# Performance work log

Measured on AMD Instinct MI355X. Metric: run time of the kernel, lower is better.

Reference implementation:

```python
import jax, jax.numpy as jnp
import numpy as np

B, L, D = 4, 1024, 1024
H = 16
HD = D // H
SCALE = HD ** -0.5
LOCAL_WINDOW = 32
HALF = LOCAL_WINDOW // 2
TEMP = 1.0
PATTERN_TEMP = 1.0
THRESHOLD = 0.1
SPARSITY_RATIO = 0.3
# k for learned sparse topk (eval mode, static given L)
EFF = min(SPARSITY_RATIO, 1.0 - 10.0 / L)
K_TOP = max(1, min(L, int(L * (1.0 - EFF))))


def setup_inputs() -> dict:
    key = jax.random.key(0)
    ks = jax.random.split(key, 16)
    def xavier(k, shape, gain=1.0):
        fan_in, fan_out = shape[1], shape[0]
        a = gain * np.sqrt(6.0 / (fan_in + fan_out))
        return jax.random.uniform(k, shape, jnp.float32, -a, a)
    return {
        'x': jax.random.normal(ks[0], (B, L, D), jnp.float32),
        'w_qkv': xavier(ks[1], (3 * D, D), gain=1.0 / np.sqrt(2.0)),
        'w_proj': xavier(ks[2], (D, D)),
        'b_proj': jnp.zeros((D,), jnp.float32),
        'ps_w1': xavier(ks[3], (D, D), gain=0.5),
        'ps_b1': jnp.zeros((D,), jnp.float32),
        'ln_g': jnp.ones((D,), jnp.float32),
        'ln_b': jnp.zeros((D,), jnp.float32),
        'ps_w2': xavier(ks[4], (D // 2, D), gain=0.5),
        'ps_b2': jnp.zeros((D // 2,), jnp.float32),
        'ps_w3': xavier(ks[5], (3, D // 2), gain=0.5),
        'ps_b3': jnp.zeros((3,), jnp.float32),
        'pattern_bias': jnp.array([0.05, 0.0, -0.05], jnp.float32),
        'sparse_w': jax.random.normal(ks[6], (H, 1, 1), jnp.float32) * 0.1 + 1.0,
        'sparse_b': jnp.zeros((H, 1, 1), jnp.float32),
    }


def _forward(x, w_qkv, w_proj, b_proj, ps_w1, ps_b1, ln_g, ln_b,
             ps_w2, ps_b2, ps_w3, ps_b3, pattern_bias, sparse_w, sparse_b):
    qkv = (x @ w_qkv.T).reshape(B, L, 3, H, HD)
    qkv = jnp.transpose(qkv, (2, 0, 3, 1, 4))  # [3,B,H,L,HD]
    q, k, v = qkv[0], qkv[1], qkv[2]
    scores = jnp.einsum('bhid,bhjd->bhij', q, k) * SCALE  # [B,H,L,L]

    # pattern selector on pooled features
    pooled = (jnp.mean(x, axis=1) + jnp.max(x, axis=1)) / 2.0  # [B,D]
    h = pooled @ ps_w1.T + ps_b1
    mu = jnp.mean(h, axis=-1, keepdims=True)
    var = jnp.mean((h - mu) ** 2, axis=-1, keepdims=True)
    h = (h - mu) / jnp.sqrt(var + 1e-5) * ln_g + ln_b
    h = jax.nn.gelu(h, approximate=False)
    h = jax.nn.gelu(h @ ps_w2.T + ps_b2, approximate=False)
    logits = h @ ps_w3.T + ps_b3 + pattern_bias  # [B,3]
    pw = jax.nn.softmax(logits / PATTERN_TEMP, axis=-1)  # [B,3]

    # learned sparse mask via per-head affine + topk scatter
    s2 = scores * jnp.abs(sparse_w)[None] + sparse_b[None]  # [B,H,L,L]
    _, topk_idx = jax.lax.top_k(s2, K_TOP)  # [B,H,L,K]
    bi = jnp.arange(B)[:, None, None, None]
    hi = jnp.arange(H)[None, :, None, None]
    li = jnp.arange(L)[None, None, :, None]
    sparse_mask = jnp.zeros_like(scores).at[bi, hi, li, topk_idx].set(1.0)

    # local sliding-window mask |i-j| <= HALF
    i = jnp.arange(L)
    local = (jnp.abs(i[:, None] - i[None, :]) <= HALF).astype(jnp.float32)  # [L,L]

    combined = (pw[:, 0, None, None, None] * local[None, None]
                + pw[:, 1, None, None, None]
                + pw[:, 2, None, None, None] * sparse_mask)
    binary = combined > THRESHOLD
    scores = jnp.where(binary, scores, -jnp.inf)

    # fallback: rows fully masked attend only to themselves (score 0)
    all_masked = ~jnp.any(binary, axis=-1)  # [B,H,L]
    eye = jnp.eye(L, dtype=bool)
    scores = jnp.where(all_masked[..., None] & eye[None, None], 0.0, scores)

    attn = jax.nn.softmax(scores / TEMP, axis=-1)
    out = jnp.einsum('bhij,bhjd->bhid', attn, v)  # [B,H,L,HD]
    out = jnp.transpose(out, (0, 2, 1, 3)).reshape(B, L, D)
    return out @ w_proj.T + b_proj


def reference(x, w_qkv, w_proj, b_proj, ps_w1, ps_b1, ln_g, ln_b,
              ps_w2, ps_b2, ps_w3, ps_b3, pattern_bias, sparse_w, sparse_b):
    return _forward(x, w_qkv, w_proj, b_proj, ps_w1, ps_b1, ln_g, ln_b,
                    ps_w2, ps_b2, ps_w3, ps_b3, pattern_bias, sparse_w, sparse_b)
```

## Files before the change

### kernel.cpp

```cpp
#include <hip/hip_runtime.h>
#include <math.h>

#define KTOP_ 716
#define SCALE_ 0.125f
#define QSCALE_ 0.1803368801111731f
#define LN2_ 0.6931471805599453f

#define WAIT_VMCNT(n) asm volatile("s_waitcnt vmcnt(" #n ")" ::: "memory")
static __device__ inline void SBAR() {
  __builtin_amdgcn_sched_barrier(0);
  __builtin_amdgcn_s_barrier();
  __builtin_amdgcn_sched_barrier(0);
}

typedef float f4v __attribute__((ext_vector_type(4)));
typedef short s8v __attribute__((ext_vector_type(8)));
typedef __bf16 bf8v __attribute__((ext_vector_type(8)));

static __device__ inline unsigned short f2bf(float f) {
  unsigned u = __float_as_uint(f);
  u += 0x7fffu + ((u >> 16) & 1u);
  return (unsigned short)(u >> 16);
}
static __device__ inline unsigned short f2bfn(float f) {
  union { __bf16 b; unsigned short u; } cv;
  cv.b = (__bf16)f;
  return cv.u;
}
static __device__ inline float bf2f(unsigned short h) {
  return __uint_as_float((unsigned)h << 16);
}
static __device__ inline f4v mfma16(s8v a, s8v b, f4v c) {
  union { s8v s; bf8v b; } ua, ub;
  ua.s = a; ub.s = b;
  return __builtin_amdgcn_mfma_f32_16x16x32_bf16(ua.b, ub.b, c, 0, 0, 0);
}
static __device__ inline void gload16(const unsigned short* g, unsigned short* lbase) {
  __builtin_amdgcn_global_load_lds(
      (const __attribute__((address_space(1))) unsigned int*)g,
      (__attribute__((address_space(3))) unsigned int*)lbase, 16, 0, 0);
}

__global__ __launch_bounds__(256) void pool1(const float* __restrict__ x,
                                             float* __restrict__ psum,
                                             float* __restrict__ pmax,
                                             unsigned short* __restrict__ xs) {
  int bid = blockIdx.x;
  int b = bid >> 6, sl = bid & 63;
  int t = threadIdx.x;
  float s[4] = {0.f, 0.f, 0.f, 0.f};
  float m[4] = {-INFINITY, -INFINITY, -INFINITY, -INFINITY};
  const float* xb = x + ((size_t)b << 20) + (size_t)sl * 16 * 1024;
  unsigned short* xo = xs + ((size_t)(b * 1024 + sl * 16)) * 1024;
  for (int l = 0; l < 16; ++l) {
    #pragma unroll
    for (int dg = 0; dg < 4; ++dg) {
      float v = xb[l * 1024 + dg * 256 + t];
      s[dg] += v;
      m[dg] = fmaxf(m[dg], v);
      xo[(size_t)l * 1024 + dg * 256 + t] = f2bfn(v);
    }
  }
  #pragma unroll
  for (int dg = 0; dg < 4; ++dg) {
    psum[(size_t)bid * 1024 + dg * 256 + t] = s[dg];
    pmax[(size_t)bid * 1024 + dg * 256 + t] = m[dg];
  }
}

__global__ __launch_bounds__(256) void ps_gemv1(const float* __restrict__ psum,
                                                const float* __restrict__ pmax,
                                                const float* __restrict__ w1,
                                                const float* __restrict__ b1,
                                                float* __restrict__ h1) {
  __shared__ float pool_s[1024];
  int bid = blockIdx.x;
  int b = bid >> 4, og = bid & 15;
  int t = threadIdx.x;
  #pragma unroll
  for (int i = 0; i < 4; ++i) {
    int d = t + 256 * i;
    float s = 0.f, m = -INFINITY;
    #pragma unroll 8
    for (int sl = 0; sl < 64; ++sl) {
      s += psum[((size_t)b * 64 + sl) * 1024 + d];
      m = fmaxf(m, pmax[((size_t)b * 64 + sl) * 1024 + d]);
    }
    pool_s[d] = (s * (1.0f / 1024.0f) + m) * 0.5f;
  }
  __syncthreads();
  int ol = t >> 2, ks = t & 3;
  int o = og * 64 + ol;
  const float4* wr = (const float4*)(w1 + (size_t)o * 1024 + ks * 256);
  const float4* pp = (const float4*)(&pool_s[ks * 256]);
  float acc = 0.f;
  #pragma unroll 8
  for (int j = 0; j < 64; ++j) {
    float4 a = wr[j], p = pp[j];
    acc += a.x * p.x + a.y * p.y + a.z * p.z + a.w * p.w;
  }
  acc += __shfl_xor(acc, 1, 64);
  acc += __shfl_xor(acc, 2, 64);
  if (ks == 0) h1[b * 1024 + o] = acc + b1[o];
}

__global__ __launch_bounds__(256) void ps_gemv2(const float* __restrict__ h1,
                                                const float* __restrict__ lng,
                                                const float* __restrict__ lnb,
                                                const float* __restrict__ w2,
                                                const float* __restrict__ b2,
                                                float* __restrict__ h2) {
  __shared__ float hs[1024];
  __shared__ float red[256];
  int bid = blockIdx.x;
  int b = bid >> 3, og = bid & 7;
  int t = threadIdx.x;
  const float* hb = h1 + b * 1024;
  float v0[4];
  float ls = 0.f;
  #pragma unroll
  for (int i = 0; i < 4; ++i) { v0[i] = hb[t + 256 * i]; ls += v0[i]; }
  red[t] = ls; __syncthreads();
  for (int s = 128; s > 0; s >>= 1) { if (t < s) red[t] += red[t + s]; __syncthreads(); }
  float mean = red[0] * (1.0f / 1024.0f);
  __syncthreads();
  float lq = 0.f;
  #pragma unroll
  for (int i = 0; i < 4; ++i) { float dv = v0[i] - mean; lq += dv * dv; }
  red[t] = lq; __syncthreads();
  for (int s = 128; s > 0; s >>= 1) { if (t < s) red[t] += red[t + s]; __syncthreads(); }
  float rstd = 1.0f / sqrtf(red[0] * (1.0f / 1024.0f) + 1e-5f);
  #pragma unroll
  for (int i = 0; i < 4; ++i) {
    float v = (v0[i] - mean) * rstd * lng[t + 256 * i] + lnb[t + 256 * i];
    hs[t + 256 * i] = 0.5f * v * (1.0f + erff(v * 0.70710678118654752f));
  }
  __syncthreads();
  int ol = t >> 2, ks = t & 3;
  int o = og * 64 + ol;
  const float4* wr = (const float4*)(w2 + (size_t)o * 1024 + ks * 256);
  const float4* pp = (const float4*)(&hs[ks * 256]);
  float acc = 0.f;
  #pragma unroll 8
  for (int j = 0; j < 64; ++j) {
    float4 a = wr[j], p = pp[j];
    acc += a.x * p.x + a.y * p.y + a.z * p.z + a.w * p.w;
  }
  acc += __shfl_xor(acc, 1, 64);
  acc += __shfl_xor(acc, 2, 64);
  if (ks == 0) {
    float v = acc + b2[o];
    h2[b * 512 + o] = 0.5f * v * (1.0f + erff(v * 0.70710678118654752f));
  }
}

__global__ __launch_bounds__(256) void ps_logits(const float* __restrict__ h2,
                                                 const float* __restrict__ w3,
                                                 const float* __restrict__ b3,
                                                 const float* __restrict__ pb,
                                                 int* __restrict__ meta) {
  __shared__ float red[256];
  int b = blockIdx.x, t = threadIdx.x;
  float lgv[3];
  for (int c = 0; c < 3; ++c) {
    float p = 0.f;
    for (int i = t; i < 512; i += 256) p += h2[b * 512 + i] * w3[c * 512 + i];
    red[t] = p; __syncthreads();
    for (int s = 128; s > 0; s >>= 1) { if (t < s) red[t] += red[t + s]; __syncthreads(); }
    lgv[c] = red[0] + b3[c] + pb[c];
    __syncthreads();
  }
  if (t == 0) {
    float mx = fmaxf(lgv[0], fmaxf(lgv[1], lgv[2]));
    float e0 = __expf(lgv[0] - mx), e1 = __expf(lgv[1] - mx), e2 = __expf(lgv[2] - mx);
    float inv = 1.0f / (e0 + e1 + e2);
    float p0 = e0 * inv, p1 = e1 * inv, p2 = e2 * inv;
    float c00 = p1;
    float c10 = p0 + p1;
    float c01 = p1 + p2;
    float c11 = (p0 + p1) + p2;
    int t00 = c00 > 0.1f, t10 = c10 > 0.1f, t01 = c01 > 0.1f, t11 = c11 > 0.1f;
    meta[b * 8 + 0] = t00;
    meta[b * 8 + 1] = t10;
    meta[b * 8 + 2] = t01;
    meta[b * 8 + 3] = t11;
    meta[b * 8 + 4] = (t00 != t01) || (t10 != t11);
  }
}

__global__ __launch_bounds__(256) void prep_w(const float* __restrict__ w_qkv,
                                              const float* __restrict__ w_proj,
                                              unsigned short* __restrict__ wqs,
                                              unsigned short* __restrict__ wps) {
  int i = blockIdx.x * 256 + threadIdx.x;
  const float* src;
  unsigned short* dst;
  int idx;
  if (i < 786432) { src = w_qkv; dst = wqs; idx = i; }
  else            { src = w_proj; dst = wps; idx = i - 786432; }
  float4 v = ((const float4*)src)[idx];
  ushort4 o;
  o.x = f2bfn(v.x); o.y = f2bfn(v.y); o.z = f2bfn(v.z); o.w = f2bfn(v.w);
  *(ushort4*)(dst + (size_t)idx * 4) = o;
}

template <int MODE, int TM>
__global__ __launch_bounds__(256) void gemm_sp(
    const unsigned short* __restrict__ A, const unsigned short* __restrict__ B,
    const float* __restrict__ bias,
    unsigned short* __restrict__ qxo, unsigned short* __restrict__ kxo,
    unsigned short* __restrict__ vxo,
    float* __restrict__ out, int Nb) {
  constexpr int MFR = TM / 32;
  __shared__ unsigned short AsmA[TM * 64];
  __shared__ unsigned short AsmB[TM * 64];
  __shared__ unsigned short BsmA[128 * 64];
  __shared__ unsigned short BsmB[128 * 64];

  int bid = blockIdx.x;
  int bm, bn;
  if (MODE == 0) {
    int xcd = bid & 7, idx = bid >> 3;
    int rb = (xcd >> 1) * 8, cb = (xcd & 1) * 12;
    int r, c;
    if (idx < 64) { r = idx & 7; c = idx >> 3; }
    else          { int j = idx - 64; r = j & 7; c = 8 + (j >> 3); }
    bm = rb + r; bn = cb + c;
  } else {
    int cpx = gridDim.x >> 3;
    int g = (bid & 7) * cpx + (bid >> 3);
    bm = g / Nb; bn = g % Nb;
  }
  size_t row0 = (size_t)bm * TM, col0 = (size_t)bn * 128;

  int tid = threadIdx.x, lane = tid & 63, wv = tid >> 6;
  int wm = (wv >> 1) * (MFR * 16), wn = (wv & 1) << 6;
  int rowg = lane >> 4, colc = lane & 15;

  f4v acc[MFR][4];
  #pragma unroll
  for (int mf = 0; mf < MFR; ++mf)
    #pragma unroll
    for (int nf = 0; nf < 4; ++nf) acc[mf][nf] = (f4v){0.f, 0.f, 0.f, 0.f};

  const unsigned short* Abase = A + row0 * 1024;
  const unsigned short* Bbase = B + col0 * 1024;

  auto STAGE = [&](int kb, unsigned short* Ad, unsigned short* Bd) {
    #pragma unroll
    for (int p = 0; p < TM / 32; ++p) {
      int idx = p * 256 + tid;
      int row = idx >> 3;
      int sc = (idx & 7) ^ (row & 7);
      gload16(Abase + (size_t)row * 1024 + kb + sc * 8,
              Ad + (size_t)(p * 256 + wv * 64) * 8);
    }
    #pragma unroll
    for (int p = 0; p < 4; ++p) {
      int idx = p * 256 + tid;
      int row = idx >> 3;
      int sc = (idx & 7) ^ (row & 7);
      gload16(Bbase + (size_t)row * 1024 + kb + sc * 8,
              Bd + (size_t)(p * 256 + wv * 64) * 8);
    }
  };

  auto COMPUTE = [&](const unsigned short* Ab, const unsigned short* Bb) {
    #pragma unroll
    for (int ks = 0; ks < 2; ++ks) {
      s8v af[MFR], bf_[4];
      #pragma unroll
      for (int mf = 0; mf < MFR; ++mf) {
        int row = wm + mf * 16 + colc;
        int kby = (ks * 64 + rowg * 16) ^ ((row & 7) << 4);
        af[mf] = *(const s8v*)((const char*)Ab + row * 128 + kby);
      }
      #pragma unroll
      for (int nf = 0; nf < 4; ++nf) {
        int row = wn + nf * 16 + colc;
        int kby = (ks * 64 + rowg * 16) ^ ((row & 7) << 4);
        bf_[nf] = *(const s8v*)((const char*)Bb + row * 128 + kby);
      }
      __builtin_amdgcn_s_setprio(1);
      #pragma unroll
      for (int mf = 0; mf < MFR; ++mf)
        #pragma unroll
        for (int nf = 0; nf < 4; ++nf)
          acc[mf][nf] = mfma16(af[mf], bf_[nf], acc[mf][nf]);
      __builtin_amdgcn_s_setprio(0);
    }
  };

  STAGE(0, AsmA, BsmA);
  for (int kb = 0; kb < 1024; kb += 128) {
    STAGE(kb + 64, AsmB, BsmB);
    if constexpr (TM == 128) WAIT_VMCNT(8); else WAIT_VMCNT(6);
    SBAR();
    COMPUTE(AsmA, BsmA);
    SBAR();
    if (kb + 128 < 1024) {
      STAGE(kb + 128, AsmA, BsmA);
      if constexpr (TM == 128) WAIT_VMCNT(8); else WAIT_VMCNT(6);
    } else {
      WAIT_VMCNT(0);
    }
    SBAR();
    COMPUTE(AsmB, BsmB);
    SBAR();
  }

  if (MODE == 0) {
    int c = (int)(col0 >> 10);
    #pragma unroll
    for (int mf = 0; mf < MFR; ++mf) {
      int m0 = (int)row0 + wm + mf * 16 + rowg * 4;
      int bb = m0 >> 10, l0 = m0 & 1023;
      #pragma unroll
      for (int nf = 0; nf < 4; ++nf) {
        int n = (int)col0 + wn + nf * 16 + colc;
        int hh = (n >> 6) & 15, hd = n & 63;
        int bhl = bb * 16 + hh;
        if (c == 2) {
          ushort4 h4;
          h4.x = f2bfn(acc[mf][nf][0]);
          h4.y = f2bfn(acc[mf][nf][1]);
          h4.z = f2bfn(acc[mf][nf][2]);
          h4.w = f2bfn(acc[mf][nf][3]);
          *(ushort4*)(vxo + ((size_t)bhl * 64 + hd) * 1024 + l0) = h4;
        } else {
          unsigned short* dst = ((c == 0) ? qxo : kxo) +
                                ((size_t)bhl * 1024 + l0) * 64 + hd;
          float sc_ = (c == 0) ? QSCALE_ : 1.0f;
          #pragma unroll
          for (int r = 0; r < 4; ++r)
            dst[(size_t)r * 64] = f2bfn(acc[mf][nf][r] * sc_);
        }
      }
    }
  } else {
    #pragma unroll
    for (int mf = 0; mf < MFR; ++mf) {
      #pragma unroll
      for (int r = 0; r < 4; ++r) {
        int m = (int)row0 + wm + mf * 16 + rowg * 4 + r;
        #pragma unroll
        for (int nf = 0; nf < 4; ++nf) {
          int n = (int)col0 + wn + nf * 16 + colc;
          out[(size_t)m * 1024 + n] = acc[mf][nf][r] + bias[n];
        }
      }
    }
  }
}

__global__ __launch_bounds__(512) void attn_flash(
    const unsigned short* __restrict__ qx, const unsigned short* __restrict__ kx,
    const unsigned short* __restrict__ vx, const int* __restrict__ meta,
    unsigned short* __restrict__ ao) {
  int n = blockIdx.x;
  int bh = ((n & 7) << 3) | (n >> 6);
  int qt2 = (n >> 3) & 7;
  int b = bh >> 4, h = bh & 15;
  const int* mb = meta + b * 8;
  if (mb[4]) return;
  int t00 = mb[0], t10 = mb[1];

  int tid = threadIdx.x, lane = tid & 63, wv = tid >> 6;
  int g = lane >> 4, colc = lane & 15;
  int bq0 = qt2 * 128;
  int q0 = bq0 + wv * 16;

  if (!t10) {
    #pragma unroll
    for (int it = 0; it < 4; ++it) {
      int idx = tid + it * 512;
      int r = idx >> 4, dc = (idx & 15) * 4;
      ushort4 o;
      unsigned short* op = (unsigned short*)&o;
      #pragma unroll
      for (int j = 0; j < 4; ++j)
        op[j] = vx[((size_t)bh * 64 + dc + j) * 1024 + bq0 + r];
      *(ushort4*)(ao + ((size_t)b * 1024 + bq0 + r) * 1024 + h * 64 + dc) = o;
    }
    return;
  }
  bool local_only = !t00;

  __shared__ __align__(16) unsigned short KsmA[64 * 64];
  __shared__ __align__(16) unsigned short KsmB[64 * 64];
  __shared__ __align__(16) unsigned short VsmA[64 * 64];
  __shared__ __align__(16) unsigned short VsmB[64 * 64];
  __shared__ __align__(16) unsigned short px[8][16][64];

  const unsigned short* qb = qx + ((size_t)bh * 1024 + q0 + colc) * 64 + g * 8;
  s8v Q0 = *(const s8v*)(qb);
  s8v Q1 = *(const s8v*)(qb + 32);

  f4v O[4];
  #pragma unroll
  for (int df = 0; df < 4; ++df) O[df] = (f4v){0.f, 0.f, 0.f, 0.f};
  float m = -1e30f, lsum = 0.f;

  const unsigned short* kxb = kx + ((size_t)bh << 10) * 64;
  const unsigned short* vxb = vx + ((size_t)bh << 16);

  int jb_lo = 0, jb_hi = 15;
  if (local_only) {
    int lo = (bq0 - 16) >> 6, hi = (bq0 + 143) >> 6;
    jb_lo = lo < 0 ? 0 : lo;
    jb_hi = hi > 15 ? 15 : hi;
  }

  int srow = tid >> 3;
  int ssc = (tid & 7) ^ (srow & 7);
  auto STAGE = [&](int jb2, unsigned short* Kd, unsigned short* Vd) {
    int jc = jb2 << 6;
    unsigned short* lbase_k = Kd + (size_t)(wv * 64) * 8;
    unsigned short* lbase_v = Vd + (size_t)(wv * 64) * 8;
    gload16(kxb + (size_t)(jc + srow) * 64 + ssc * 8, lbase_k);
    gload16(vxb + (size_t)srow * 1024 + jc + ssc * 8, lbase_v);
  };

  int swk = (colc & 7) << 4;
  int sx = (colc & 7) << 1;

  auto COMPUTE = [&](int jc0, const char* Kb, const char* Vb) {
    if (local_only && (jc0 + 63 < q0 - 16 || jc0 > q0 + 31)) return;
    f4v s[4];
    __builtin_amdgcn_s_setprio(1);
    #pragma unroll
    for (int jf = 0; jf < 4; ++jf) {
      const char* kp = Kb + (jf * 16 + colc) * 128;
      s8v K0 = *(const s8v*)(kp + ((g * 16) ^ swk));
      s8v K1 = *(const s8v*)(kp + ((64 + g * 16) ^ swk));
      f4v acc = (f4v){0.f, 0.f, 0.f, 0.f};
      acc = mfma16(K0, Q0, acc);
      acc = mfma16(K1, Q1, acc);
      s[jf] = acc;
    }
    __builtin_amdgcn_s_setprio(0);

    if (local_only) {
      int i = q0 + colc;
      #pragma unroll
      for (int jf = 0; jf < 4; ++jf)
        #pragma unroll
        for (int r = 0; r < 4; ++r) {
          int j = jc0 + jf * 16 + 4 * g + r;
          int dj = i - j;
          if (dj > 16 || dj < -16) s[jf][r] = -1e30f;
        }
    }

    float cm = fmaxf(
        fmaxf(fmaxf(fmaxf(s[0][0], s[0][1]), fmaxf(s[0][2], s[0][3])),
              fmaxf(fmaxf(s[1][0], s[1][1]), fmaxf(s[1][2], s[1][3]))),
        fmaxf(fmaxf(fmaxf(s[2][0], s[2][1]), fmaxf(s[2][2], s[2][3])),
              fmaxf(fmaxf(s[3][0], s[3][1]), fmaxf(s[3][2], s[3][3]))));
    cm = fmaxf(cm, __shfl_xor(cm, 16, 64));
    cm = fmaxf(cm, __shfl_xor(cm, 32, 64));

    if (__any(cm > m + 8.0f)) {
      float mn = fmaxf(m, cm);
      float fac = __builtin_amdgcn_exp2f(m - mn);
      m = mn;
      lsum *= fac;
      float fo[4];
      #pragma unroll
      for (int r = 0; r < 4; ++r)
        fo[r] = __shfl(fac, (lane & 48) + g * 4 + r, 64);
      #pragma unroll
      for (int df = 0; df < 4; ++df)
        #pragma unroll
        for (int r = 0; r < 4; ++r) O[df][r] *= fo[r];
    }

    float psum = 0.f;
    #pragma unroll
    for (int jf = 0; jf < 4; ++jf) {
      float p0 = __builtin_amdgcn_exp2f(s[jf][0] - m);
      float p1 = __builtin_amdgcn_exp2f(s[jf][1] - m);
      float p2 = __builtin_amdgcn_exp2f(s[jf][2] - m);
      float p3 = __builtin_amdgcn_exp2f(s[jf][3] - m);
      psum += (p0 + p1) + (p2 + p3);
      ushort4 pk;
      pk.x = f2bfn(p0); pk.y = f2bfn(p1); pk.z = f2bfn(p2); pk.w = f2bfn(p3);
      *(ushort4*)&px[wv][colc][4 * ((jf * 4 + g) ^ sx)] = pk;
    }
    psum += __shfl_xor(psum, 16, 64);
    psum += __shfl_xor(psum, 32, 64);
    lsum += psum;

    s8v Pf[2];
    #pragma unroll
    for (int ks = 0; ks < 2; ++ks)
      Pf[ks] = *(const s8v*)&px[wv][colc][4 * ((ks * 8 + 2 * g) ^ sx)];
    __builtin_amdgcn_s_setprio(1);
    #pragma unroll
    for (int df = 0; df < 4; ++df) {
      const char* vp = Vb + (df * 16 + colc) * 128;
      #pragma unroll
      for (int ks = 0; ks < 2; ++ks) {
        s8v Vf = *(const s8v*)(vp + ((ks * 64 + g * 16) ^ swk));
        O[df] = mfma16(Pf[ks], Vf, O[df]);
      }
    }
    __builtin_amdgcn_s_setprio(0);
  };

  STAGE(jb_lo, KsmA, VsmA);
  int jb = jb_lo;
  while (true) {
    if (jb + 1 <= jb_hi) { STAGE(jb + 1, KsmB, VsmB); WAIT_VMCNT(2); }
    else                 { WAIT_VMCNT(0); }
    SBAR();
    COMPUTE(jb << 6, (const char*)KsmA, (const char*)VsmA);
    SBAR();
    if (++jb > jb_hi) break;
    if (jb + 1 <= jb_hi) { STAGE(jb + 1, KsmA, VsmA); WAIT_VMCNT(2); }
    else                 { WAIT_VMCNT(0); }
    SBAR();
    COMPUTE(jb << 6, (const char*)KsmB, (const char*)VsmB);
    SBAR();
    if (++jb > jb_hi) break;
  }

  float linv[4];
  #pragma unroll
  for (int r = 0; r < 4; ++r)
    linv[r] = 1.0f / __shfl(lsum, (lane & 48) + g * 4 + r, 64);
  #pragma unroll
  for (int df = 0; df < 4; ++df) {
    #pragma unroll
    for (int r = 0; r < 4; ++r) {
      int i = q0 + g * 4 + r;
      ao[((size_t)b * 1024 + i) * 1024 + h * 64 + df * 16 + colc] =
          f2bfn(O[df][r] * linv[r]);
    }
  }
}

__global__ __launch_bounds__(256) void attn_sparse(
    const unsigned short* __restrict__ qx, const unsigned short* __restrict__ kx,
    const unsigned short* __restrict__ vx, const int* __restrict__ meta,
    unsigned short* __restrict__ ao) {
  __shared__ float S[32][1028];
  __shared__ float qs[32][68];
  __shared__ float kc[64][68];
  __shared__ float rowsum_s[32];

  int tid = threadIdx.x;
  int lane = tid & 63;
  int wv = tid >> 6;
  int id = blockIdx.x;
  int rt = id & 31;
  int h = (id >> 5) & 15;
  int b = id >> 9;
  int bh = b * 16 + h;
  int row0 = rt * 32;

  const int* mb = meta + b * 8;
  int t00 = mb[0], t10 = mb[1], t01 = mb[2], t11 = mb[3], needs = mb[4];
  if (!needs) return;

  #pragma unroll
  for (int i = 0; i < 8; ++i) {
    int idx = tid + 256 * i;
    int r = idx >> 6, d = idx & 63;
    qs[r][d] = bf2f(qx[((size_t)bh * 1024 + row0 + r) * 64 + d]);
  }

  int lr = lane >> 4, lc = lane & 15;
  int r_a = wv * 8 + lr * 2;
  int r_b = r_a + 1;

  for (int cb = 0; cb < 16; ++cb) {
    __syncthreads();
    #pragma unroll
    for (int i = 0; i < 2; ++i) {
      int idx = tid + 256 * i;
      int cc = idx >> 3, d0 = (idx & 7) * 8;
      union { s8v v; unsigned short u[8]; } kv8;
      kv8.v = *(const s8v*)(kx + ((size_t)bh * 1024 + cb * 64 + cc) * 64 + d0);
      #pragma unroll
      for (int j = 0; j < 8; ++j) kc[cc][d0 + j] = bf2f(kv8.u[j]);
    }
    __syncthreads();

    float acc0[4] = {0.f, 0.f, 0.f, 0.f};
    float acc1[4] = {0.f, 0.f, 0.f, 0.f};
    for (int dq = 0; dq < 64; dq += 4) {
      float4 qa = *(const float4*)&qs[r_a][dq];
      float4 qb = *(const float4*)&qs[r_b][dq];
      #pragma unroll
      for (int cj = 0; cj < 4; ++cj) {
        float4 kv = *(const float4*)&kc[lc + 16 * cj][dq];
        acc0[cj] += qa.x * kv.x + qa.y * kv.y + qa.z * kv.z + qa.w * kv.w;
        acc1[cj] += qb.x * kv.x + qb.y * kv.y + qb.z * kv.z + qb.w * kv.w;
      }
    }
    #pragma unroll
    for (int cj = 0; cj < 4; ++cj) {
      S[r_a][cb * 64 + lc + 16 * cj] = acc0[cj] * LN2_;
      S[r_b][cb * 64 + lc + 16 * cj] = acc1[cj] * LN2_;
    }
  }

  for (int rr = 0; rr < 8; ++rr) {
    int r = wv * 8 + rr;
    int grow = row0 + r;
    float sv[16];
    unsigned kv[16];
    #pragma unroll
    for (int i2 = 0; i2 < 16; ++i2) {
      float s = S[r][lane + 64 * i2];
      sv[i2] = s;
      unsigned u = __float_as_uint(s);
      kv[i2] = (u & 0x80000000u) ? ~u : (u | 0x80000000u);
    }
    unsigned T = 0u;
    for (int bit = 31; bit >= 0; --bit) {
      unsigned cand = T | (1u << bit);
      int cnt = 0;
      #pragma unroll
      for (int i2 = 0; i2 < 16; ++i2) cnt += (kv[i2] >= cand) ? 1 : 0;
      for (int off = 32; off; off >>= 1) cnt += __shfl_xor(cnt, off, 64);
      if (cnt >= KTOP_) T = cand;
    }
    float mx = -INFINITY;
    int kept = 0;
    unsigned kmask = 0;
    #pragma unroll
    for (int i2 = 0; i2 < 16; ++i2) {
      int j = lane + 64 * i2;
      int sp = (kv[i2] >= T) ? 1 : 0;
      int dj = grow - j;
      int lo = (dj <= 16 && dj >= -16) ? 1 : 0;
      int keep = sp ? (lo ? t11 : t01) : (lo ? t10 : t00);
      kept += keep;
      if (keep) { kmask |= (1u << i2); mx = fmaxf(mx, sv[i2]); }
    }
    for (int off = 32; off; off >>= 1) {
      mx = fmaxf(mx, __shfl_xor(mx, off, 64));
      kept += __shfl_xor(kept, off, 64);
    }
    if (kept == 0) {
      #pragma unroll
      for (int i2 = 0; i2 < 16; ++i2) {
        int j = lane + 64 * i2;
        S[r][j] = (j == grow) ? 1.0f : 0.0f;
      }
      if (lane == 0) rowsum_s[r] = 1.0f;
    } else {
      float sum = 0.f;
      #pragma unroll
      for (int i2 = 0; i2 < 16; ++i2) {
        float p = ((kmask >> i2) & 1u) ? __expf(sv[i2] - mx) : 0.0f;
        sum += p;
        S[r][lane + 64 * i2] = p;
      }
      for (int off = 32; off; off >>= 1) sum += __shfl_xor(sum, off, 64);
      if (lane == 0) rowsum_s[r] = sum;
    }
  }

  int ld = lane & 15;
  int d0 = ld * 4;
  float4 oa0 = make_float4(0.f, 0.f, 0.f, 0.f);
  float4 oa1 = make_float4(0.f, 0.f, 0.f, 0.f);
  for (int vb = 0; vb < 16; ++vb) {
    __syncthreads();
    #pragma unroll
    for (int i = 0; i < 2; ++i) {
      int idx = tid + 256 * i;
      int d = idx >> 3, c0 = (idx & 7) * 8;
      union { s8v v; unsigned short u[8]; } vv8;
      vv8.v = *(const s8v*)(vx + ((size_t)bh * 64 + d) * 1024 + vb * 64 + c0);
      #pragma unroll
      for (int j = 0; j < 8; ++j) kc[c0 + j][d] = bf2f(vv8.u[j]);
    }
    __syncthreads();
    for (int cq = 0; cq < 64; cq += 4) {
      float4 pa = *(const float4*)&S[r_a][vb * 64 + cq];
      float4 pb = *(const float4*)&S[r_b][vb * 64 + cq];
      float par[4] = {pa.x, pa.y, pa.z, pa.w};
      float pbr[4] = {pb.x, pb.y, pb.z, pb.w};
      #pragma unroll
      for (int tt = 0; tt < 4; ++tt) {
        float4 vv = *(const float4*)&kc[cq + tt][d0];
        oa0.x += par[tt] * vv.x; oa0.y += par[tt] * vv.y;
        oa0.z += par[tt] * vv.z; oa0.w += par[tt] * vv.w;
        oa1.x += pbr[tt] * vv.x; oa1.y += pbr[tt] * vv.y;
        oa1.z += pbr[tt] * vv.z; oa1.w += pbr[tt] * vv.w;
      }
    }
  }
  float inv0 = 1.0f / rowsum_s[r_a];
  float inv1 = 1.0f / rowsum_s[r_b];
  ushort4 o0, o1;
  unsigned short* o0p = (unsigned short*)&o0;
  unsigned short* o1p = (unsigned short*)&o1;
  float v0[4] = {oa0.x * inv0, oa0.y * inv0, oa0.z * inv0, oa0.w * inv0};
  float v1[4] = {oa1.x * inv1, oa1.y * inv1, oa1.z * inv1, oa1.w * inv1};
  #pragma unroll
  for (int j = 0; j < 4; ++j) {
    o0p[j] = f2bf(v0[j]);
    o1p[j] = f2bf(v1[j]);
  }
  *(ushort4*)(ao + ((size_t)b * 1024 + row0 + r_a) * 1024 + h * 64 + d0) = o0;
  *(ushort4*)(ao + ((size_t)b * 1024 + row0 + r_b) * 1024 + h * 64 + d0) = o1;
}

__global__ __launch_bounds__(256) void pool_kernel(const float* __restrict__ x,
                                                   float* __restrict__ pooled) {
  int g = blockIdx.x * 256 + threadIdx.x;
  int b = g >> 10, d = g & 1023;
  const float* xp = x + ((size_t)b << 20) + d;
  float s = 0.f, m = -INFINITY;
  #pragma unroll 4
  for (int l = 0; l < 1024; ++l) {
    float v = xp[(size_t)l << 10];
    s += v;
    m = fmaxf(m, v);
  }
  pooled[g] = (s * (1.0f / 1024.0f) + m) * 0.5f;
}

__global__ __launch_bounds__(256) void qkv_gemm(const float* __restrict__ X,
                                                const float* __restrict__ W,
                                                float* __restrict__ qw,
                                                float* __restrict__ kw,
                                                float* __restrict__ vw) {
  __shared__ float As[8][128];
  __shared__ float Bs[8][128];
  int tid = threadIdx.x;
  int row0 = blockIdx.y * 128, col0 = blockIdx.x * 128;
  int lr = tid >> 1;
  int lk = (tid & 1) * 4;
  int ty = tid >> 4, tx = tid & 15;
  float acc[8][8] = {};

  for (int kb = 0; kb < 1024; kb += 8) {
    float4 a4 = *(const float4*)(X + (size_t)(row0 + lr) * 1024 + kb + lk);
    float4 b4 = *(const float4*)(W + (size_t)(col0 + lr) * 1024 + kb + lk);
    __syncthreads();
    As[lk + 0][lr] = a4.x; As[lk + 1][lr] = a4.y; As[lk + 2][lr] = a4.z; As[lk + 3][lr] = a4.w;
    Bs[lk + 0][lr] = b4.x; Bs[lk + 1][lr] = b4.y; Bs[lk + 2][lr] = b4.z; Bs[lk + 3][lr] = b4.w;
    __syncthreads();
    #pragma unroll
    for (int kk = 0; kk < 8; ++kk) {
      float av[8], bv[8];
      #pragma unroll
      for (int i = 0; i < 8; ++i) av[i] = As[kk][ty * 8 + i];
      #pragma unroll
      for (int j = 0; j < 8; ++j) bv[j] = Bs[kk][tx * 8 + j];
      #pragma unroll
      for (int i = 0; i < 8; ++i)
        #pragma unroll
        for (int j = 0; j < 8; ++j) acc[i][j] += av[i] * bv[j];
    }
  }
  #pragma unroll
  for (int i = 0; i < 8; ++i) {
    int m = row0 + ty * 8 + i;
    int bb = m >> 10, l = m & 1023;
    #pragma unroll
    for (int j = 0; j < 8; j += 4) {
      int n = col0 + tx * 8 + j;
      int c = n >> 10;
      int hh = (n >> 6) & 15;
      int hd = n & 63;
      float* base = (c == 0) ? qw : (c == 1) ? kw : vw;
      float* dst = base + ((size_t)(bb * 16 + hh) * 1024 + l) * 64 + hd;
      *(float4*)dst = make_float4(acc[i][j], acc[i][j + 1], acc[i][j + 2], acc[i][j + 3]);
    }
  }
}

__global__ __launch_bounds__(256) void proj_gemm(const float* __restrict__ A,
                                                 const float* __restrict__ W,
                                                 const float* __restrict__ bias,
                                                 float* __restrict__ out) {
  __shared__ float As[8][128];
  __shared__ float Bs[8][128];
  int tid = threadIdx.x;
  int row0 = blockIdx.y * 128, col0 = blockIdx.x * 128;
  int lr = tid >> 1;
  int lk = (tid & 1) * 4;
  int ty = tid >> 4, tx = tid & 15;
  float acc[8][8] = {};

  for (int kb = 0; kb < 1024; kb += 8) {
    float4 a4 = *(const float4*)(A + (size_t)(row0 + lr) * 1024 + kb + lk);
    float4 b4 = *(const float4*)(W + (size_t)(col0 + lr) * 1024 + kb + lk);
    __syncthreads();
    As[lk + 0][lr] = a4.x; As[lk + 1][lr] = a4.y; As[lk + 2][lr] = a4.z; As[lk + 3][lr] = a4.w;
    Bs[lk + 0][lr] = b4.x; Bs[lk + 1][lr] = b4.y; Bs[lk + 2][lr] = b4.z; Bs[lk + 3][lr] = b4.w;
    __syncthreads();
    #pragma unroll
    for (int kk = 0; kk < 8; ++kk) {
      float av[8], bv[8];
      #pragma unroll
      for (int i = 0; i < 8; ++i) av[i] = As[kk][ty * 8 + i];
      #pragma unroll
      for (int j = 0; j < 8; ++j) bv[j] = Bs[kk][tx * 8 + j];
      #pragma unroll
      for (int i = 0; i < 8; ++i)
        #pragma unroll
        for (int j = 0; j < 8; ++j) acc[i][j] += av[i] * bv[j];
    }
  }
  #pragma unroll
  for (int i = 0; i < 8; ++i) {
    int m = row0 + ty * 8 + i;
    #pragma unroll
    for (int j = 0; j < 8; j += 4) {
      int n = col0 + tx * 8 + j;
      *(float4*)(out + (size_t)m * 1024 + n) =
          make_float4(acc[i][j] + bias[n], acc[i][j + 1] + bias[n + 1],
                      acc[i][j + 2] + bias[n + 2], acc[i][j + 3] + bias[n + 3]);
    }
  }
}

__global__ __launch_bounds__(256) void pattern_kernel(
    const float* __restrict__ pooled,
    const float* __restrict__ w1, const float* __restrict__ b1,
    const float* __restrict__ lng, const float* __restrict__ lnb,
    const float* __restrict__ w2, const float* __restrict__ b2,
    const float* __restrict__ w3, const float* __restrict__ b3,
    const float* __restrict__ pb, int* __restrict__ meta) {
  __shared__ float pool_s[1024];
  __shared__ float h1[1024];
  __shared__ float h2[512];
  __shared__ float red[256];
  int b = blockIdx.x, t = threadIdx.x;

  for (int i = t; i < 1024; i += 256) pool_s[i] = pooled[b * 1024 + i];
  __syncthreads();
  for (int o = t; o < 1024; o += 256) {
    float acc = b1[o];
    const float* wr = w1 + (size_t)o * 1024;
    for (int k = 0; k < 1024; ++k) acc += pool_s[k] * wr[k];
    h1[o] = acc;
  }
  __syncthreads();
  float ls = 0.f;
  for (int i = t; i < 1024; i += 256) ls += h1[i];
  red[t] = ls; __syncthreads();
  for (int s = 128; s > 0; s >>= 1) { if (t < s) red[t] += red[t + s]; __syncthreads(); }
  float mean = red[0] * (1.0f / 1024.0f);
  __syncthreads();
  float lq = 0.f;
  for (int i = t; i < 1024; i += 256) { float dv = h1[i] - mean; lq += dv * dv; }
  red[t] = lq; __syncthreads();
  for (int s = 128; s > 0; s >>= 1) { if (t < s) red[t] += red[t + s]; __syncthreads(); }
  float var = red[0] * (1.0f / 1024.0f);
  float rstd = 1.0f / sqrtf(var + 1e-5f);
  __syncthreads();
  for (int i = t; i < 1024; i += 256) {
    float v = (h1[i] - mean) * rstd * lng[i] + lnb[i];
    h1[i] = 0.5f * v * (1.0f + erff(v * 0.70710678118654752f));
  }
  __syncthreads();
  for (int o = t; o < 512; o += 256) {
    float acc = b2[o];
    const float* wr = w2 + (size_t)o * 1024;
    for (int k = 0; k < 1024; ++k) acc += h1[k] * wr[k];
    h2[o] = 0.5f * acc * (1.0f + erff(acc * 0.70710678118654752f));
  }
  __syncthreads();
  float lgv[3];
  for (int c = 0; c < 3; ++c) {
    float p = 0.f;
    for (int i = t; i < 512; i += 256) p += h2[i] * w3[c * 512 + i];
    __syncthreads();
    red[t] = p; __syncthreads();
    for (int s = 128; s > 0; s >>= 1) { if (t < s) red[t] += red[t + s]; __syncthreads(); }
    lgv[c] = red[0] + b3[c] + pb[c];
  }
  if (t == 0) {
    float mx = fmaxf(lgv[0], fmaxf(lgv[1], lgv[2]));
    float e0 = __expf(lgv[0] - mx), e1 = __expf(lgv[1] - mx), e2 = __expf(lgv[2] - mx);
    float inv = 1.0f / (e0 + e1 + e2);
    float p0 = e0 * inv, p1 = e1 * inv, p2 = e2 * inv;
    float c00 = p1;
    float c10 = p0 + p1;
    float c01 = p1 + p2;
    float c11 = (p0 + p1) + p2;
    int t00 = c00 > 0.1f, t10 = c10 > 0.1f, t01 = c01 > 0.1f, t11 = c11 > 0.1f;
    meta[b * 8 + 0] = t00;
    meta[b * 8 + 1] = t10;
    meta[b * 8 + 2] = t01;
    meta[b * 8 + 3] = t11;
    meta[b * 8 + 4] = (t00 != t01) || (t10 != t11);
  }
}

__global__ __launch_bounds__(256) void attn_kernel_f32(const float* __restrict__ qw,
                                                       const float* __restrict__ kw,
                                                       const float* __restrict__ vw,
                                                       const int* __restrict__ meta,
                                                       float* __restrict__ ao) {
  __shared__ float S[32][1028];
  __shared__ float qs[32][68];
  __shared__ float kc[64][68];
  __shared__ float rowsum_s[32];

  int tid = threadIdx.x;
  int lane = tid & 63;
  int wv = tid >> 6;
  int id = blockIdx.x;
  int rt = id & 31;
  int h = (id >> 5) & 15;
  int b = id >> 9;
  int bh = b * 16 + h;
  int row0 = rt * 32;

  const int* mb = meta + b * 8;
  int t00 = mb[0], t10 = mb[1], t01 = mb[2], t11 = mb[3], needs = mb[4];

  {
    const float4* qp = (const float4*)(qw + ((size_t)bh * 1024 + row0 + wv * 8) * 64);
    #pragma unroll
    for (int i = 0; i < 2; ++i) {
      int f = lane + 64 * i;
      float4 v = qp[f];
      int r = wv * 8 + (f >> 4);
      int d = (f & 15) << 2;
      qs[r][d] = v.x; qs[r][d + 1] = v.y; qs[r][d + 2] = v.z; qs[r][d + 3] = v.w;
    }
  }

  int lr = lane >> 4, lc = lane & 15;
  int r_a = wv * 8 + lr * 2;
  int r_b = r_a + 1;

  for (int cb = 0; cb < 16; ++cb) {
    __syncthreads();
    const float4* kp = (const float4*)(kw + ((size_t)bh * 1024 + cb * 64) * 64);
    #pragma unroll
    for (int i = 0; i < 4; ++i) {
      int f = tid + 256 * i;
      float4 v = kp[f];
      int c = f >> 4, d = (f & 15) << 2;
      kc[c][d] = v.x; kc[c][d + 1] = v.y; kc[c][d + 2] = v.z; kc[c][d + 3] = v.w;
    }
    __syncthreads();

    float acc0[4] = {0.f, 0.f, 0.f, 0.f};
    float acc1[4] = {0.f, 0.f, 0.f, 0.f};
    for (int dq = 0; dq < 64; dq += 4) {
      float4 qa = *(const float4*)&qs[r_a][dq];
      float4 qb = *(const float4*)&qs[r_b][dq];
      #pragma unroll
      for (int cj = 0; cj < 4; ++cj) {
        float4 kv = *(const float4*)&kc[lc + 16 * cj][dq];
        acc0[cj] += qa.x * kv.x + qa.y * kv.y + qa.z * kv.z + qa.w * kv.w;
        acc1[cj] += qb.x * kv.x + qb.y * kv.y + qb.z * kv.z + qb.w * kv.w;
      }
    }
    #pragma unroll
    for (int cj = 0; cj < 4; ++cj) {
      S[r_a][cb * 64 + lc + 16 * cj] = acc0[cj] * SCALE_;
      S[r_b][cb * 64 + lc + 16 * cj] = acc1[cj] * SCALE_;
    }
  }

  for (int rr = 0; rr < 8; ++rr) {
    int r = wv * 8 + rr;
    int grow = row0 + r;
    float sv[16];
    unsigned kv[16];
    #pragma unroll
    for (int i2 = 0; i2 < 16; ++i2) {
      float s = S[r][lane + 64 * i2];
      sv[i2] = s;
      unsigned u = __float_as_uint(s);
      kv[i2] = (u & 0x80000000u) ? ~u : (u | 0x80000000u);
    }
    unsigned T = 0u;
    if (needs) {
      for (int bit = 31; bit >= 0; --bit) {
        unsigned cand = T | (1u << bit);
        int cnt = 0;
        #pragma unroll
        for (int i2 = 0; i2 < 16; ++i2) cnt += (kv[i2] >= cand) ? 1 : 0;
        for (int off = 32; off; off >>= 1) cnt += __shfl_xor(cnt, off, 64);
        if (cnt >= KTOP_) T = cand;
      }
    }
    float mx = -INFINITY;
    int kept = 0;
    unsigned kmask = 0;
    #pragma unroll
    for (int i2 = 0; i2 < 16; ++i2) {
      int j = lane + 64 * i2;
      int sp = (kv[i2] >= T) ? 1 : 0;
      int dj = grow - j;
      int lo = (dj <= 16 && dj >= -16) ? 1 : 0;
      int keep = sp ? (lo ? t11 : t01) : (lo ? t10 : t00);
      kept += keep;
      if (keep) { kmask |= (1u << i2); mx = fmaxf(mx, sv[i2]); }
    }
    for (int off = 32; off; off >>= 1) {
      mx = fmaxf(mx, __shfl_xor(mx, off, 64));
      kept += __shfl_xor(kept, off, 64);
    }
    if (kept == 0) {
      #pragma unroll
      for (int i2 = 0; i2 < 16; ++i2) {
        int j = lane + 64 * i2;
        S[r][j] = (j == grow) ? 1.0f : 0.0f;
      }
      if (lane == 0) rowsum_s[r] = 1.0f;
    } else {
      float sum = 0.f;
      #pragma unroll
      for (int i2 = 0; i2 < 16; ++i2) {
        float p = ((kmask >> i2) & 1u) ? __expf(sv[i2] - mx) : 0.0f;
        sum += p;
        S[r][lane + 64 * i2] = p;
      }
      for (int off = 32; off; off >>= 1) sum += __shfl_xor(sum, off, 64);
      if (lane == 0) rowsum_s[r] = sum;
    }
  }

  int ld = lane & 15;
  int d0 = ld * 4;
  float4 oa0 = make_float4(0.f, 0.f, 0.f, 0.f);
  float4 oa1 = make_float4(0.f, 0.f, 0.f, 0.f);
  for (int vb = 0; vb < 16; ++vb) {
    __syncthreads();
    const float4* vp = (const float4*)(vw + ((size_t)bh * 1024 + vb * 64) * 64);
    #pragma unroll
    for (int i = 0; i < 4; ++i) {
      int f = tid + 256 * i;
      float4 v = vp[f];
      int c = f >> 4, d = (f & 15) << 2;
      kc[c][d] = v.x; kc[c][d + 1] = v.y; kc[c][d + 2] = v.z; kc[c][d + 3] = v.w;
    }
    __syncthreads();
    for (int cq = 0; cq < 64; cq += 4) {
      float4 pa = *(const float4*)&S[r_a][vb * 64 + cq];
      float4 pb = *(const float4*)&S[r_b][vb * 64 + cq];
      float par[4] = {pa.x, pa.y, pa.z, pa.w};
      float pbr[4] = {pb.x, pb.y, pb.z, pb.w};
      #pragma unroll
      for (int tt = 0; tt < 4; ++tt) {
        float4 vv = *(const float4*)&kc[cq + tt][d0];
        oa0.x += par[tt] * vv.x; oa0.y += par[tt] * vv.y;
        oa0.z += par[tt] * vv.z; oa0.w += par[tt] * vv.w;
        oa1.x += pbr[tt] * vv.x; oa1.y += pbr[tt] * vv.y;
        oa1.z += pbr[tt] * vv.z; oa1.w += pbr[tt] * vv.w;
      }
    }
  }
  float inv0 = 1.0f / rowsum_s[r_a];
  float inv1 = 1.0f / rowsum_s[r_b];
  float* p0 = ao + ((size_t)b * 1024 + row0 + r_a) * 1024 + h * 64 + d0;
  float* p1 = ao + ((size_t)b * 1024 + row0 + r_b) * 1024 + h * 64 + d0;
  *(float4*)p0 = make_float4(oa0.x * inv0, oa0.y * inv0, oa0.z * inv0, oa0.w * inv0);
  *(float4*)p1 = make_float4(oa1.x * inv1, oa1.y * inv1, oa1.z * inv1, oa1.w * inv1);
}

extern "C" void kernel_launch(void* const* d_in, const int* in_sizes, int n_in,
                              void* d_out, int out_size, void* d_ws, size_t ws_size,
                              hipStream_t stream) {
  const float* x      = (const float*)d_in[0];
  const float* w_qkv  = (const float*)d_in[1];
  const float* w_proj = (const float*)d_in[2];
  const float* b_proj = (const float*)d_in[3];
  const float* ps_w1  = (const float*)d_in[4];
  const float* ps_b1  = (const float*)d_in[5];
  const float* ln_g   = (const float*)d_in[6];
  const float* ln_b   = (const float*)d_in[7];
  const float* ps_w2  = (const float*)d_in[8];
  const float* ps_b2  = (const float*)d_in[9];
  const float* ps_w3  = (const float*)d_in[10];
  const float* ps_b3  = (const float*)d_in[11];
  const float* pbias  = (const float*)d_in[12];

  float* ws = (float*)d_ws;
  float* pooled = ws;
  int*   meta   = (int*)(ws + 4096);
  float* h1buf  = ws + 8192;
  float* h2buf  = ws + 12288;
  float* ppsum  = ws + 16384;
  float* ppmax  = ws + 278528;
  float* qw = ws + 1048576;
  float* kw = qw + 4194304;
  float* vw = kw + 4194304;
  float* ao = vw + 4194304;
  unsigned short* u16b = (unsigned short*)(ao + 4194304);
  unsigned short* xs   = u16b;
  unsigned short* wqs  = xs + 4194304;
  unsigned short* wps  = wqs + 3145728;
  unsigned short* aos  = wps + 1048576;
  unsigned short* qx   = aos + 4194304;
  unsigned short* kx   = qx + 4194304;
  unsigned short* vx   = kx + 4194304;
  float* out = (float*)d_out;

  const size_t NEED_FULL = (size_t)(1048576 + 4 * 4194304) * 4 +
                           (size_t)(4194304 + 3145728 + 1048576 + 4194304 +
                                    3 * 4194304) * 2;

  if (ws_size >= NEED_FULL) {
    pool1<<<256, 256, 0, stream>>>(x, ppsum, ppmax, xs);
    ps_gemv1<<<64, 256, 0, stream>>>(ppsum, ppmax, ps_w1, ps_b1, h1buf);
    ps_gemv2<<<32, 256, 0, stream>>>(h1buf, ln_g, ln_b, ps_w2, ps_b2, h2buf);
    ps_logits<<<4, 256, 0, stream>>>(h2buf, ps_w3, ps_b3, pbias, meta);

    prep_w<<<4096, 256, 0, stream>>>(w_qkv, w_proj, wqs, wps);
    gemm_sp<0, 128><<<768, 256, 0, stream>>>(xs, wqs, nullptr, qx, kx, vx,
                                             nullptr, 24);

    attn_flash<<<512, 512, 0, stream>>>(qx, kx, vx, meta, aos);
    attn_sparse<<<2048, 256, 0, stream>>>(qx, kx, vx, meta, aos);

    gemm_sp<1, 64><<<512, 256, 0, stream>>>(aos, wps, b_proj,
                                            nullptr, nullptr, nullptr, out, 8);
  } else {
    pool_kernel<<<16, 256, 0, stream>>>(x, pooled);
    pattern_kernel<<<4, 256, 0, stream>>>(pooled, ps_w1, ps_b1, ln_g, ln_b,
                                          ps_w2, ps_b2, ps_w3, ps_b3, pbias, meta);
    qkv_gemm<<<dim3(24, 32), 256, 0, stream>>>(x, w_qkv, qw, kw, vw);
    attn_kernel_f32<<<2048, 256, 0, stream>>>(qw, kw, vw, meta, ao);
    proj_gemm<<<dim3(8, 32), 256, 0, stream>>>(ao, w_proj, b_proj, out);
  }
}
```

Measured before the change: 135.9 us.

## Widen QKV GEMM tiles to 128x192 and double flash-attention KV tile to 128

The QKV GEMM becomes templated on tile width and runs 128x192 tiles on 512 blocks instead of 128x128 on 768. That improves operand reuse and fits one wave of blocks, but raises per-block register and LDS use. The Q/K/V head is now chosen per column in the epilogue, since a tile can span the Q/K boundary. The flash attention kernel stages 128-key K/V tiles with a 16-way V swizzle and processes P·V in two 64-key halves, halving the loop iterations and barriers at the cost of more LDS per block.

Result: slower. 142.3 us (+4.7%).

```diff
diff --git a/kernel.cpp b/kernel.cpp
--- a/kernel.cpp
+++ b/kernel.cpp
@@ -204,7 +204,7 @@
   *(ushort4*)(dst + (size_t)idx * 4) = o;
 }
 
-template <int MODE, int TM>
+template <int MODE, int TM, int TN>
 __global__ __launch_bounds__(256) void gemm_sp(
     const unsigned short* __restrict__ A, const unsigned short* __restrict__ B,
     const float* __restrict__ bias,
@@ -212,36 +212,34 @@
     unsigned short* __restrict__ vxo,
     float* __restrict__ out, int Nb) {
   constexpr int MFR = TM / 32;
+  constexpr int NFR = TN / 32;
   __shared__ unsigned short AsmA[TM * 64];
   __shared__ unsigned short AsmB[TM * 64];
-  __shared__ unsigned short BsmA[128 * 64];
-  __shared__ unsigned short BsmB[128 * 64];
+  __shared__ unsigned short BsmA[TN * 64];
+  __shared__ unsigned short BsmB[TN * 64];
 
   int bid = blockIdx.x;
   int bm, bn;
   if (MODE == 0) {
     int xcd = bid & 7, idx = bid >> 3;
-    int rb = (xcd >> 1) * 8, cb = (xcd & 1) * 12;
-    int r, c;
-    if (idx < 64) { r = idx & 7; c = idx >> 3; }
-    else          { int j = idx - 64; r = j & 7; c = 8 + (j >> 3); }
-    bm = rb + r; bn = cb + c;
+    bm = (xcd >> 1) * 8 + (idx & 7);
+    bn = (xcd & 1) * 8 + (idx >> 3);
   } else {
     int cpx = gridDim.x >> 3;
     int g = (bid & 7) * cpx + (bid >> 3);
     bm = g / Nb; bn = g % Nb;
   }
-  size_t row0 = (size_t)bm * TM, col0 = (size_t)bn * 128;
+  size_t row0 = (size_t)bm * TM, col0 = (size_t)bn * TN;
 
   int tid = threadIdx.x, lane = tid & 63, wv = tid >> 6;
-  int wm = (wv >> 1) * (MFR * 16), wn = (wv & 1) << 6;
+  int wm = (wv >> 1) * (MFR * 16), wn = (wv & 1) * (NFR * 16);
   int rowg = lane >> 4, colc = lane & 15;
 
-  f4v acc[MFR][4];
+  f4v acc[MFR][NFR];
   #pragma unroll
   for (int mf = 0; mf < MFR; ++mf)
     #pragma unroll
-    for (int nf = 0; nf < 4; ++nf) acc[mf][nf] = (f4v){0.f, 0.f, 0.f, 0.f};
+    for (int nf = 0; nf < NFR; ++nf) acc[mf][nf] = (f4v){0.f, 0.f, 0.f, 0.f};
 
   const unsigned short* Abase = A + row0 * 1024;
   const unsigned short* Bbase = B + col0 * 1024;
@@ -256,7 +254,7 @@
               Ad + (size_t)(p * 256 + wv * 64) * 8);
     }
     #pragma unroll
-    for (int p = 0; p < 4; ++p) {
+    for (int p = 0; p < TN / 32; ++p) {
       int idx = p * 256 + tid;
       int row = idx >> 3;
       int sc = (idx & 7) ^ (row & 7);
@@ -268,7 +266,7 @@
   auto COMPUTE = [&](const unsigned short* Ab, const unsigned short* Bb) {
     #pragma unroll
     for (int ks = 0; ks < 2; ++ks) {
-      s8v af[MFR], bf_[4];
+      s8v af[MFR], bf_[NFR];
       #pragma unroll
       for (int mf = 0; mf < MFR; ++mf) {
         int row = wm + mf * 16 + colc;
@@ -276,7 +274,7 @@
         af[mf] = *(const s8v*)((const char*)Ab + row * 128 + kby);
       }
       #pragma unroll
-      for (int nf = 0; nf < 4; ++nf) {
+      for (int nf = 0; nf < NFR; ++nf) {
         int row = wn + nf * 16 + colc;
         int kby = (ks * 64 + rowg * 16) ^ ((row & 7) << 4);
         bf_[nf] = *(const s8v*)((const char*)Bb + row * 128 + kby);
@@ -285,22 +283,24 @@
       #pragma unroll
       for (int mf = 0; mf < MFR; ++mf)
         #pragma unroll
-        for (int nf = 0; nf < 4; ++nf)
+        for (int nf = 0; nf < NFR; ++nf)
           acc[mf][nf] = mfma16(af[mf], bf_[nf], acc[mf][nf]);
       __builtin_amdgcn_s_setprio(0);
     }
   };
+
+  constexpr int NLD = TM / 32 + TN / 32;
 
   STAGE(0, AsmA, BsmA);
   for (int kb = 0; kb < 1024; kb += 128) {
     STAGE(kb + 64, AsmB, BsmB);
-    if constexpr (TM == 128) WAIT_VMCNT(8); else WAIT_VMCNT(6);
+    if constexpr (NLD == 10) WAIT_VMCNT(10); else WAIT_VMCNT(6);
     SBAR();
     COMPUTE(AsmA, BsmA);
     SBAR();
     if (kb + 128 < 1024) {
       STAGE(kb + 128, AsmA, BsmA);
-      if constexpr (TM == 128) WAIT_VMCNT(8); else WAIT_VMCNT(6);
+      if constexpr (NLD == 10) WAIT_VMCNT(10); else WAIT_VMCNT(6);
     } else {
       WAIT_VMCNT(0);
     }
@@ -310,14 +310,14 @@
   }
 
   if (MODE == 0) {
-    int c = (int)(col0 >> 10);
     #pragma unroll
     for (int mf = 0; mf < MFR; ++mf) {
       int m0 = (int)row0 + wm + mf * 16 + rowg * 4;
       int bb = m0 >> 10, l0 = m0 & 1023;
       #pragma unroll
-      for (int nf = 0; nf < 4; ++nf) {
+      for (int nf = 0; nf < NFR; ++nf) {
         int n = (int)col0 + wn + nf * 16 + colc;
+        int c = n >> 10;
         int hh = (n >> 6) & 15, hd = n & 63;
         int bhl = bb * 16 + hh;
         if (c == 2) {
@@ -344,7 +344,7 @@
       for (int r = 0; r < 4; ++r) {
         int m = (int)row0 + wm + mf * 16 + rowg * 4 + r;
         #pragma unroll
-        for (int nf = 0; nf < 4; ++nf) {
+        for (int nf = 0; nf < NFR; ++nf) {
           int n = (int)col0 + wn + nf * 16 + colc;
           out[(size_t)m * 1024 + n] = acc[mf][nf][r] + bias[n];
         }
@@ -386,10 +386,10 @@
   }
   bool local_only = !t00;
 
-  __shared__ __align__(16) unsigned short KsmA[64 * 64];
-  __shared__ __align__(16) unsigned short KsmB[64 * 64];
-  __shared__ __align__(16) unsigned short VsmA[64 * 64];
-  __shared__ __align__(16) unsigned short VsmB[64 * 64];
+  __shared__ __align__(16) unsigned short KsmA[128 * 64];
+  __shared__ __align__(16) unsigned short KsmB[128 * 64];
+  __shared__ __align__(16) unsigned short VsmA[64 * 128];
+  __shared__ __align__(16) unsigned short VsmB[64 * 128];
   __shared__ __align__(16) unsigned short px[8][16][64];
 
   const unsigned short* qb = qx + ((size_t)bh * 1024 + q0 + colc) * 64 + g * 8;
@@ -404,32 +404,39 @@
   const unsigned short* kxb = kx + ((size_t)bh << 10) * 64;
   const unsigned short* vxb = vx + ((size_t)bh << 16);
 
-  int jb_lo = 0, jb_hi = 15;
+  int jt_lo = 0, jt_hi = 7;
   if (local_only) {
-    int lo = (bq0 - 16) >> 6, hi = (bq0 + 143) >> 6;
-    jb_lo = lo < 0 ? 0 : lo;
-    jb_hi = hi > 15 ? 15 : hi;
-  }
-
-  int srow = tid >> 3;
-  int ssc = (tid & 7) ^ (srow & 7);
-  auto STAGE = [&](int jb2, unsigned short* Kd, unsigned short* Vd) {
-    int jc = jb2 << 6;
-    unsigned short* lbase_k = Kd + (size_t)(wv * 64) * 8;
-    unsigned short* lbase_v = Vd + (size_t)(wv * 64) * 8;
-    gload16(kxb + (size_t)(jc + srow) * 64 + ssc * 8, lbase_k);
-    gload16(vxb + (size_t)srow * 1024 + jc + ssc * 8, lbase_v);
+    int lo = (bq0 - 16) >> 7, hi = (bq0 + 143) >> 7;
+    jt_lo = lo < 0 ? 0 : lo;
+    jt_hi = hi > 7 ? 7 : hi;
+  }
+
+  auto STAGE = [&](int jt, unsigned short* Kd, unsigned short* Vd) {
+    int jc = jt << 7;
+    #pragma unroll
+    for (int p = 0; p < 2; ++p) {
+      int cidx = p * 512 + tid;
+      int krow = cidx >> 3;
+      int ksc = (cidx & 7) ^ (krow & 7);
+      gload16(kxb + (size_t)(jc + krow) * 64 + ksc * 8,
+              Kd + (size_t)(p * 512 + wv * 64) * 8);
+      int vrow = cidx >> 4;
+      int vsc = (cidx & 15) ^ (vrow & 15);
+      gload16(vxb + (size_t)vrow * 1024 + jc + vsc * 8,
+              Vd + (size_t)(p * 512 + wv * 64) * 8);
+    }
   };
 
   int swk = (colc & 7) << 4;
+  int swv = colc << 4;
   int sx = (colc & 7) << 1;
 
   auto COMPUTE = [&](int jc0, const char* Kb, const char* Vb) {
-    if (local_only && (jc0 + 63 < q0 - 16 || jc0 > q0 + 31)) return;
-    f4v s[4];
+    if (local_only && (jc0 + 127 < q0 - 16 || jc0 > q0 + 31)) return;
+    f4v s[8];
     __builtin_amdgcn_s_setprio(1);
     #pragma unroll
-    for (int jf = 0; jf < 4; ++jf) {
+    for (int jf = 0; jf < 8; ++jf) {
       const char* kp = Kb + (jf * 16 + colc) * 128;
       s8v K0 = *(const s8v*)(kp + ((g * 16) ^ swk));
       s8v K1 = *(const s8v*)(kp + ((64 + g * 16) ^ swk));
@@ -443,7 +450,7 @@
     if (local_only) {
       int i = q0 + colc;
       #pragma unroll
-      for (int jf = 0; jf < 4; ++jf)
+      for (int jf = 0; jf < 8; ++jf)
         #pragma unroll
         for (int r = 0; r < 4; ++r) {
           int j = jc0 + jf * 16 + 4 * g + r;
@@ -452,11 +459,11 @@
         }
     }
 
-    float cm = fmaxf(
-        fmaxf(fmaxf(fmaxf(s[0][0], s[0][1]), fmaxf(s[0][2], s[0][3])),
-              fmaxf(fmaxf(s[1][0], s[1][1]), fmaxf(s[1][2], s[1][3]))),
-        fmaxf(fmaxf(fmaxf(s[2][0], s[2][1]), fmaxf(s[2][2], s[2][3])),
-              fmaxf(fmaxf(s[3][0], s[3][1]), fmaxf(s[3][2], s[3][3]))));
+    float cm = -1e30f;
+    #pragma unroll
+    for (int jf = 0; jf < 8; ++jf)
+      #pragma unroll
+      for (int r = 0; r < 4; ++r) cm = fmaxf(cm, s[jf][r]);
     cm = fmaxf(cm, __shfl_xor(cm, 16, 64));
     cm = fmaxf(cm, __shfl_xor(cm, 32, 64));
 
@@ -477,52 +484,55 @@
 
     float psum = 0.f;
     #pragma unroll
-    for (int jf = 0; jf < 4; ++jf) {
-      float p0 = __builtin_amdgcn_exp2f(s[jf][0] - m);
-      float p1 = __builtin_amdgcn_exp2f(s[jf][1] - m);
-      float p2 = __builtin_amdgcn_exp2f(s[jf][2] - m);
-      float p3 = __builtin_amdgcn_exp2f(s[jf][3] - m);
-      psum += (p0 + p1) + (p2 + p3);
-      ushort4 pk;
-      pk.x = f2bfn(p0); pk.y = f2bfn(p1); pk.z = f2bfn(p2); pk.w = f2bfn(p3);
-      *(ushort4*)&px[wv][colc][4 * ((jf * 4 + g) ^ sx)] = pk;
+    for (int hf = 0; hf < 2; ++hf) {
+      #pragma unroll
+      for (int j4 = 0; j4 < 4; ++j4) {
+        int jf = hf * 4 + j4;
+        float p0 = __builtin_amdgcn_exp2f(s[jf][0] - m);
+        float p1 = __builtin_amdgcn_exp2f(s[jf][1] - m);
+        float p2 = __builtin_amdgcn_exp2f(s[jf][2] - m);
+        float p3 = __builtin_amdgcn_exp2f(s[jf][3] - m);
+        psum += (p0 + p1) + (p2 + p3);
+        ushort4 pk;
+        pk.x = f2bfn(p0); pk.y = f2bfn(p1); pk.z = f2bfn(p2); pk.w = f2bfn(p3);
+        *(ushort4*)&px[wv][colc][4 * ((j4 * 4 + g) ^ sx)] = pk;
+      }
+      s8v Pf[2];
+      #pragma unroll
+      for (int ks = 0; ks < 2; ++ks)
+        Pf[ks] = *(const s8v*)&px[wv][colc][4 * ((ks * 8 + 2 * g) ^ sx)];
+      __builtin_amdgcn_s_setprio(1);
+      #pragma unroll
+      for (int df = 0; df < 4; ++df) {
+        const char* vp = Vb + (df * 16 + colc) * 256;
+        #pragma unroll
+        for (int ks = 0; ks < 2; ++ks) {
+          s8v Vf = *(const s8v*)(vp + ((hf * 128 + ks * 64 + g * 16) ^ swv));
+          O[df] = mfma16(Pf[ks], Vf, O[df]);
+        }
+      }
+      __builtin_amdgcn_s_setprio(0);
     }
     psum += __shfl_xor(psum, 16, 64);
     psum += __shfl_xor(psum, 32, 64);
     lsum += psum;
-
-    s8v Pf[2];
-    #pragma unroll
-    for (int ks = 0; ks < 2; ++ks)
-      Pf[ks] = *(const s8v*)&px[wv][colc][4 * ((ks * 8 + 2 * g) ^ sx)];
-    __builtin_amdgcn_s_setprio(1);
-    #pragma unroll
-    for (int df = 0; df < 4; ++df) {
-      const char* vp = Vb + (df * 16 + colc) * 128;
-      #pragma unroll
-      for (int ks = 0; ks < 2; ++ks) {
-        s8v Vf = *(const s8v*)(vp + ((ks * 64 + g * 16) ^ swk));
-        O[df] = mfma16(Pf[ks], Vf, O[df]);
-      }
-    }
-    __builtin_amdgcn_s_setprio(0);
   };
 
-  STAGE(jb_lo, KsmA, VsmA);
-  int jb = jb_lo;
+  STAGE(jt_lo, KsmA, VsmA);
+  int jt = jt_lo;
   while (true) {
-    if (jb + 1 <= jb_hi) { STAGE(jb + 1, KsmB, VsmB); WAIT_VMCNT(2); }
+    if (jt + 1 <= jt_hi) { STAGE(jt + 1, KsmB, VsmB); WAIT_VMCNT(4); }
     else                 { WAIT_VMCNT(0); }
     SBAR();
-    COMPUTE(jb << 6, (const char*)KsmA, (const char*)VsmA);
+    COMPUTE(jt << 7, (const char*)KsmA, (const char*)VsmA);
     SBAR();
-    if (++jb > jb_hi) break;
-    if (jb + 1 <= jb_hi) { STAGE(jb + 1, KsmA, VsmA); WAIT_VMCNT(2); }
+    if (++jt > jt_hi) break;
+    if (jt + 1 <= jt_hi) { STAGE(jt + 1, KsmA, VsmA); WAIT_VMCNT(4); }
     else                 { WAIT_VMCNT(0); }
     SBAR();
-    COMPUTE(jb << 6, (const char*)KsmB, (const char*)VsmB);
+    COMPUTE(jt << 7, (const char*)KsmB, (const char*)VsmB);
     SBAR();
-    if (++jb > jb_hi) break;
+    if (++jt > jt_hi) break;
   }
 
   float linv[4];
@@ -1114,14 +1124,14 @@
     ps_logits<<<4, 256, 0, stream>>>(h2buf, ps_w3, ps_b3, pbias, meta);
 
     prep_w<<<4096, 256, 0, stream>>>(w_qkv, w_proj, wqs, wps);
-    gemm_sp<0, 128><<<768, 256, 0, stream>>>(xs, wqs, nullptr, qx, kx, vx,
-                                             nullptr, 24);
+    gemm_sp<0, 128, 192><<<512, 256, 0, stream>>>(xs, wqs, nullptr, qx, kx, vx,
+                                                  nullptr, 16);
 
     attn_flash<<<512, 512, 0, stream>>>(qx, kx, vx, meta, aos);
     attn_sparse<<<2048, 256, 0, stream>>>(qx, kx, vx, meta, aos);
 
-    gemm_sp<1, 64><<<512, 256, 0, stream>>>(aos, wps, b_proj,
-                                            nullptr, nullptr, nullptr, out, 8);
+    gemm_sp<1, 64, 128><<<512, 256, 0, stream>>>(aos, wps, b_proj,
+                                                 nullptr, nullptr, nullptr, out, 8);
   } else {
     pool_kernel<<<16, 256, 0, stream>>>(x, pooled);
     pattern_kernel<<<4, 256, 0, stream>>>(pooled, ps_w1, ps_b1, ln_g, ln_b,
```
